# Kernel tuning notes

Hardware: AMD Instinct MI355X
Metric: run time of the kernel (lower is better)

## Reference

```python
import jax, jax.numpy as jnp
import numpy as np

K_F = 3          # propagation kernel
PAD_F = 1
NUM = K_F * K_F - 1   # 8 non-reference neighbors
IDX_REF = NUM // 2    # 4
PROP_TIME = 18
B, H, W = 4, 240, 1216


def _conv2d_same(x, w, b):
    # x: (B,Cin,H,W), w: (Cout,Cin,kh,kw)
    y = jax.lax.conv_general_dilated(x, w, (1, 1), 'SAME',
                                     dimension_numbers=('NCHW', 'OIHW', 'NCHW'))
    return y + b[None, :, None, None]


def _bilinear(img, y, x):
    # img: (B,H,W); y,x: (B,K,H,W) float sample coords. Zero outside bounds (DCN semantics).
    Bv, Hv, Wv = img.shape
    flat = img.reshape(Bv, -1)
    y0 = jnp.floor(y)
    x0 = jnp.floor(x)
    wy = y - y0
    wx = x - x0

    def g(yy, xx):
        valid = (yy >= 0) & (yy <= Hv - 1) & (xx >= 0) & (xx <= Wv - 1)
        yc = jnp.clip(yy, 0, Hv - 1).astype(jnp.int32)
        xc = jnp.clip(xx, 0, Wv - 1).astype(jnp.int32)
        idx = (yc * Wv + xc).reshape(Bv, -1)
        v = jnp.take_along_axis(flat, idx, axis=1).reshape(yy.shape)
        return jnp.where(valid, v, jnp.zeros((), img.dtype))

    return ((1 - wy) * (1 - wx) * g(y0, x0)
            + (1 - wy) * wx * g(y0, x0 + 1)
            + wy * (1 - wx) * g(y1 := y0 + 1, x0)
            + wy * wx * g(y1, x0 + 1))


def _deform_agg(feat, off, mask, k, pad):
    # Modulated deformable conv with w == 1, b == 0, ch_f == 1.
    # feat: (B,1,H,W); off: (B,K,2,H,W) (dy,dx); mask: (B,K,H,W)
    Bv, _, Hv, Wv = feat.shape
    kk = jnp.arange(k)
    by = (jnp.repeat(kk, k) - pad).astype(feat.dtype)  # kernel base dy, row-major
    bx = (jnp.tile(kk, k) - pad).astype(feat.dtype)    # kernel base dx
    gy = jnp.arange(Hv, dtype=feat.dtype)[None, None, :, None]
    gx = jnp.arange(Wv, dtype=feat.dtype)[None, None, None, :]
    y = gy + by[None, :, None, None] + off[:, :, 0]
    x = gx + bx[None, :, None, None] + off[:, :, 1]
    s = _bilinear(feat[:, 0], y, x)                    # (B,K,H,W)
    return jnp.sum(s * mask, axis=1, keepdims=True)


def setup_inputs() -> dict:
    key = jax.random.key(0)
    k1, k2, k3, k4, k5, k6 = jax.random.split(key, 6)
    feat_init = jax.random.uniform(k1, (B, 1, H, W), jnp.float32)
    guidance = jax.random.normal(k2, (B, 8, H, W), jnp.float32)
    confidence = jax.random.uniform(k3, (B, 1, H, W), jnp.float32)
    dep = jax.random.uniform(k4, (B, 1, H, W), jnp.float32)
    valid = (jax.random.uniform(k5, (B, 1, H, W), jnp.float32) < 0.05)
    feat_fix = dep * valid.astype(jnp.float32)
    w_oa = 0.1 * jax.random.normal(k6, (3 * NUM, 8, 3, 3), jnp.float32)
    b_oa = jnp.zeros((3 * NUM,), jnp.float32)
    aff_scale_const = jnp.full((1,), 0.5 * NUM, jnp.float32)  # gamma * num (TGASS)
    return {'feat_init': feat_init, 'guidance': guidance, 'confidence': confidence,
            'feat_fix': feat_fix, 'w_oa': w_oa, 'b_oa': b_oa,
            'aff_scale_const': aff_scale_const}


def reference(feat_init, guidance, confidence, feat_fix, w_oa, b_oa, aff_scale_const):
    Bv, _, Hv, Wv = guidance.shape
    oa = _conv2d_same(guidance, w_oa, b_oa)                 # (B,24,H,W)
    o1, o2, aff = oa[:, :NUM], oa[:, NUM:2 * NUM], oa[:, 2 * NUM:]
    # torch: cat((o1,o2),1).view(B,num,2,H,W) then insert zero ref offset at idx_ref
    off = jnp.concatenate([o1, o2], axis=1).reshape(Bv, NUM, 2, Hv, Wv)
    zeros = jnp.zeros((Bv, 1, 2, Hv, Wv), off.dtype)
    off = jnp.concatenate([off[:, :IDX_REF], zeros, off[:, IDX_REF:]], axis=1)  # (B,9,2,H,W)

    # TGASS affinity
    aff = jnp.tanh(aff) / (aff_scale_const + 1e-8)          # (B,8,H,W)

    # confidence-weighted affinity: 1x1 deform-sample of confidence at each neighbor offset
    nbr = jnp.array([0, 1, 2, 3, 5, 6, 7, 8])
    off_c = jax.lax.stop_gradient(off[:, nbr])              # (B,8,2,H,W), offsets detached
    gy = jnp.arange(Hv, dtype=aff.dtype)[None, None, :, None]
    gx = jnp.arange(Wv, dtype=aff.dtype)[None, None, None, :]
    conf_aff = _bilinear(confidence[:, 0], gy + off_c[:, :, 0], gx + off_c[:, :, 1])
    aff = aff * conf_aff

    s = jnp.sum(jnp.abs(aff), axis=1, keepdims=True) + 1e-4
    s = jnp.maximum(s, 1.0)                                 # TGASS clamp
    aff = aff / s
    aff_ref = 1.0 - jnp.sum(aff, axis=1, keepdims=True)
    aff9 = jnp.concatenate([aff[:, :IDX_REF], aff_ref, aff[:, IDX_REF:]], axis=1)  # (B,9,H,W)

    # preserve_input mask
    mask_fix = (jnp.sum((feat_fix > 0.0).astype(feat_fix.dtype), axis=1, keepdims=True) > 0.0)
    mask_fix = jax.lax.stop_gradient(mask_fix.astype(feat_fix.dtype))

    def step(feat, _):
        feat = (1.0 - mask_fix) * feat + mask_fix * feat_fix
        feat = _deform_agg(feat, off, aff9, K_F, PAD_F)
        return feat, None

    feat_result, _ = jax.lax.scan(step, feat_init, None, length=PROP_TIME)
    return feat_result, off.reshape(Bv, -1, Hv, Wv), aff9
```

## Files before the change

### kernel.cpp

```cpp
#include <hip/hip_runtime.h>
#include <hip/hip_bf16.h>

#define B_ 4
#define H_ 240
#define W_ 1216
#define HW_ (H_*W_)
#define N1_ (B_*HW_)
#define PT_ 18

__device__ __forceinline__ bool probe_bf16(const void* scale_ptr) {
    return ((const unsigned short*)scale_ptr)[0] == 0x4080;
}

__device__ __forceinline__ float ldin(const void* p, int i, bool bf) {
    if (bf) {
        unsigned int u = (unsigned int)((const unsigned short*)p)[i];
        return __uint_as_float(u << 16);
    }
    return ((const float*)p)[i];
}

__device__ __forceinline__ void stout(void* p, int i, bool bf, float v) {
    if (bf) ((__hip_bfloat16*)p)[i] = __float2bfloat16(v);
    else    ((float*)p)[i] = v;
}

__global__ __launch_bounds__(256) void k_prep_w(const void* __restrict__ w_oa,
                                                const void* __restrict__ b_oa,
                                                const void* __restrict__ scale,
                                                float* __restrict__ wc) {
    bool bf = probe_bf16(scale);
    int i = blockIdx.x * 256 + threadIdx.x;
    if (i < 1728) wc[i] = ldin(w_oa, i, bf);
    if (i < 24)   wc[1728 + i] = ldin(b_oa, i, bf);
}

__global__ __launch_bounds__(256) void k_init(const void* __restrict__ finit,
                                              const void* __restrict__ ffix,
                                              const void* __restrict__ scale,
                                              float* __restrict__ featA) {
    bool bf = probe_bf16(scale);
    int p = blockIdx.x * 256 + threadIdx.x;
    if (p >= N1_) return;
    float fx = ldin(ffix, p, bf);
    featA[p] = (fx > 0.0f) ? fx : ldin(finit, p, bf);
}

__global__ __launch_bounds__(256) void k_conv(const void* __restrict__ guid,
                                              const void* __restrict__ conf,
                                              const void* __restrict__ scale,
                                              const float* __restrict__ wc,
                                              void* __restrict__ d_out,
                                              float* __restrict__ ws_off,
                                              float* __restrict__ ws_aff,
                                              int mode2) {
    bool bf = probe_bf16(scale);
    int p = blockIdx.x * 256 + threadIdx.x;
    if (p >= N1_) return;
    int b = p / HW_;
    int r = p - b * HW_;
    int h = r / W_;
    int w = r - h * W_;

    float g[8][9];
    #pragma unroll
    for (int t = 0; t < 9; ++t) {
        int hh = h + t / 3 - 1;
        int ww = w + t % 3 - 1;
        bool v = (hh >= 0) && (hh < H_) && (ww >= 0) && (ww < W_);
        int idx0 = hh * W_ + ww;
        #pragma unroll
        for (int ci = 0; ci < 8; ++ci)
            g[ci][t] = v ? ldin(guid, (b * 8 + ci) * HW_ + idx0, bf) : 0.0f;
    }

    float oa[24];
    #pragma unroll
    for (int co = 0; co < 24; ++co) {
        float a = wc[1728 + co];
        #pragma unroll
        for (int ci = 0; ci < 8; ++ci)
            #pragma unroll
            for (int t = 0; t < 9; ++t)
                a = fmaf(g[ci][t], wc[(co * 8 + ci) * 9 + t], a);
        oa[co] = a;
    }

    float scl = ldin(scale, 0, bf);
    float inv = 1.0f / (scl + 1e-8f);

    float aft[8];
    int cbase = b * HW_;
    #pragma unroll
    for (int t = 0; t < 8; ++t) {
        float a = tanhf(oa[16 + t]) * inv;
        float y = (float)h + oa[2 * t];
        float x = (float)w + oa[2 * t + 1];
        float y0f = floorf(y), x0f = floorf(x);
        int y0 = (int)y0f, x0 = (int)x0f;
        float wy = y - y0f, wx = x - x0f;
        int y0c = min(max(y0, 0), H_ - 1), y1c = min(max(y0 + 1, 0), H_ - 1);
        int x0c = min(max(x0, 0), W_ - 1), x1c = min(max(x0 + 1, 0), W_ - 1);
        bool vy0 = (y0 >= 0) && (y0 < H_), vy1 = (y0 >= -1) && (y0 < H_ - 1);
        bool vx0 = (x0 >= 0) && (x0 < W_), vx1 = (x0 >= -1) && (x0 < W_ - 1);
        float w00 = (1.0f - wy) * (1.0f - wx); w00 = (vy0 && vx0) ? w00 : 0.0f;
        float w01 = (1.0f - wy) * wx;          w01 = (vy0 && vx1) ? w01 : 0.0f;
        float w10 = wy * (1.0f - wx);          w10 = (vy1 && vx0) ? w10 : 0.0f;
        float w11 = wy * wx;                   w11 = (vy1 && vx1) ? w11 : 0.0f;
        float f00 = ldin(conf, cbase + y0c * W_ + x0c, bf);
        float f01 = ldin(conf, cbase + y0c * W_ + x1c, bf);
        float f10 = ldin(conf, cbase + y1c * W_ + x0c, bf);
        float f11 = ldin(conf, cbase + y1c * W_ + x1c, bf);
        float cv = w00 * f00 + w01 * f01 + w10 * f10 + w11 * f11;
        aft[t] = a * cv;
    }
    float s = 1e-4f;
    #pragma unroll
    for (int t = 0; t < 8; ++t) s += fabsf(aft[t]);
    s = fmaxf(s, 1.0f);
    float rs = 1.0f / s;
    float suma = 0.0f;
    #pragma unroll
    for (int t = 0; t < 8; ++t) { aft[t] *= rs; suma += aft[t]; }
    float aref = 1.0f - suma;

    #pragma unroll
    for (int t = 0; t < 8; ++t) {
        int n9 = t + (t >= 4 ? 1 : 0);
        stout(d_out, N1_ + (b * 18 + 2 * n9)     * HW_ + r, bf, oa[2 * t]);
        stout(d_out, N1_ + (b * 18 + 2 * n9 + 1) * HW_ + r, bf, oa[2 * t + 1]);
        stout(d_out, 19 * N1_ + (b * 9 + n9) * HW_ + r, bf, aft[t]);
    }
    stout(d_out, N1_ + (b * 18 + 8) * HW_ + r, bf, 0.0f);
    stout(d_out, N1_ + (b * 18 + 9) * HW_ + r, bf, 0.0f);
    stout(d_out, 19 * N1_ + (b * 9 + 4) * HW_ + r, bf, aref);

    if (mode2) {
        #pragma unroll
        for (int t = 0; t < 8; ++t) {
            ws_off[t * N1_ + p]       = oa[2 * t];
            ws_off[(8 + t) * N1_ + p] = oa[2 * t + 1];
            int n9 = t + (t >= 4 ? 1 : 0);
            ws_aff[n9 * N1_ + p] = aft[t];
        }
        ws_aff[4 * N1_ + p] = aref;
    }
}

__global__ __launch_bounds__(256) void k_prop(const float* __restrict__ src,
                                              float* __restrict__ dst,
                                              const float* __restrict__ ws_off,
                                              const float* __restrict__ ws_aff,
                                              const void* __restrict__ d_out_all,
                                              const void* __restrict__ ffix_in,
                                              const void* __restrict__ scale,
                                              void* __restrict__ d_out_feat,
                                              int last, int mode2) {
    int p = blockIdx.x * 256 + threadIdx.x;
    if (p >= N1_) return;
    bool bf = probe_bf16(scale);
    int b = p / HW_;
    int r = p - b * HW_;
    int h = r / W_;
    int w = r - h * W_;
    const float* sp = src + b * HW_;

    float oy[8], ox[8], af[9];
    if (mode2) {
        #pragma unroll
        for (int t = 0; t < 8; ++t) {
            oy[t] = ws_off[t * N1_ + p];
            ox[t] = ws_off[(8 + t) * N1_ + p];
        }
        #pragma unroll
        for (int n = 0; n < 9; ++n) af[n] = ws_aff[n * N1_ + p];
    } else {
        #pragma unroll
        for (int t = 0; t < 8; ++t) {
            int n9 = t + (t >= 4 ? 1 : 0);
            oy[t] = ldin(d_out_all, N1_ + (b * 18 + 2 * n9)     * HW_ + r, bf);
            ox[t] = ldin(d_out_all, N1_ + (b * 18 + 2 * n9 + 1) * HW_ + r, bf);
        }
        #pragma unroll
        for (int n = 0; n < 9; ++n)
            af[n] = ldin(d_out_all, 19 * N1_ + (b * 9 + n) * HW_ + r, bf);
    }

    float acc = af[4] * sp[r];

    #pragma unroll
    for (int t = 0; t < 8; ++t) {
        int n9 = t + (t >= 4 ? 1 : 0);
        float y = (float)(h + n9 / 3 - 1) + oy[t];
        float x = (float)(w + n9 % 3 - 1) + ox[t];
        float y0f = floorf(y), x0f = floorf(x);
        int y0 = (int)y0f, x0 = (int)x0f;
        float wy = y - y0f, wx = x - x0f;
        int y0c = min(max(y0, 0), H_ - 1), y1c = min(max(y0 + 1, 0), H_ - 1);
        int x0c = min(max(x0, 0), W_ - 1), x1c = min(max(x0 + 1, 0), W_ - 1);
        bool vy0 = (y0 >= 0) && (y0 < H_), vy1 = (y0 >= -1) && (y0 < H_ - 1);
        bool vx0 = (x0 >= 0) && (x0 < W_), vx1 = (x0 >= -1) && (x0 < W_ - 1);
        float w00 = (1.0f - wy) * (1.0f - wx); w00 = (vy0 && vx0) ? w00 : 0.0f;
        float w01 = (1.0f - wy) * wx;          w01 = (vy0 && vx1) ? w01 : 0.0f;
        float w10 = wy * (1.0f - wx);          w10 = (vy1 && vx0) ? w10 : 0.0f;
        float w11 = wy * wx;                   w11 = (vy1 && vx1) ? w11 : 0.0f;
        float f00 = sp[y0c * W_ + x0c];
        float f01 = sp[y0c * W_ + x1c];
        float f10 = sp[y1c * W_ + x0c];
        float f11 = sp[y1c * W_ + x1c];
        float v = w00 * f00 + w01 * f01 + w10 * f10 + w11 * f11;
        acc = fmaf(af[n9], v, acc);
    }

    if (last) {
        stout(d_out_feat, p, probe_bf16(scale), acc);
    } else {
        float fx = ldin(ffix_in, p, bf);
        dst[p] = (fx > 0.0f) ? fx : acc;
    }
}

extern "C" void kernel_launch(void* const* d_in, const int* in_sizes, int n_in,
                              void* d_out, int out_size, void* d_ws, size_t ws_size,
                              hipStream_t stream) {
    const void* feat_init  = d_in[0];
    const void* guidance   = d_in[1];
    const void* confidence = d_in[2];
    const void* feat_fix   = d_in[3];
    const void* w_oa       = d_in[4];
    const void* b_oa       = d_in[5];
    const void* scale      = d_in[6];

    float* wsf    = (float*)d_ws;
    float* featA  = wsf;
    float* featB  = wsf + N1_;
    float* wc     = wsf + 2 * (size_t)N1_;
    float* ws_off = wsf + 2 * (size_t)N1_ + 2048;
    float* ws_aff = ws_off + 16 * (size_t)N1_;

    size_t need2 = ((size_t)27 * N1_ + 2048) * sizeof(float);
    int mode2 = (ws_size >= need2) ? 1 : 0;

    int grid = (N1_ + 255) / 256;
    hipLaunchKernelGGL(k_prep_w, dim3(7), dim3(256), 0, stream, w_oa, b_oa, scale, wc);
    hipLaunchKernelGGL(k_init, dim3(grid), dim3(256), 0, stream,
                       feat_init, feat_fix, scale, featA);
    hipLaunchKernelGGL(k_conv, dim3(grid), dim3(256), 0, stream,
                       guidance, confidence, scale, wc, d_out, ws_off, ws_aff, mode2);

    float* a = featA;
    float* bbuf = featB;
    for (int it = 0; it < PT_; ++it) {
        int last = (it == PT_ - 1) ? 1 : 0;
        hipLaunchKernelGGL(k_prop, dim3(grid), dim3(256), 0, stream,
                           a, bbuf, ws_off, ws_aff, d_out, feat_fix, scale,
                           d_out, last, mode2);
        float* t = a; a = bbuf; bbuf = t;
    }
}
```

Measured before the change: 1.017 ms.

## Pack propagation coefficients into float4 planes and restructure conv weight layout

The workspace layout for offsets, affinities and the fixed-depth value changes from 25 separate scalar planes to 7 float4 planes. Each propagation step then issues seven 16-byte loads instead of about 26 scalar loads, and it no longer reads feat_fix from the bf16/fp32 input. The conv weights are transposed to a [tap][cin][cout] layout so the conv loop accumulates all 24 outputs per loaded guidance value, without holding a 72-entry input array. The workspace requirement grows slightly, and mode2 is only taken when the workspace is large enough.

New measurement: 2.248 ms. 121% more time.

```diff
diff --git a/kernel.cpp b/kernel.cpp
--- a/kernel.cpp
+++ b/kernel.cpp
@@ -31,8 +31,14 @@
                                                 float* __restrict__ wc) {
     bool bf = probe_bf16(scale);
     int i = blockIdx.x * 256 + threadIdx.x;
-    if (i < 1728) wc[i] = ldin(w_oa, i, bf);
-    if (i < 24)   wc[1728 + i] = ldin(b_oa, i, bf);
+    if (i < 1728) {
+        int co = i / 72;
+        int rem = i - co * 72;
+        int ci = rem / 9;
+        int t = rem - ci * 9;
+        wc[(t * 8 + ci) * 24 + co] = ldin(w_oa, i, bf);
+    }
+    if (i < 24) wc[1728 + i] = ldin(b_oa, i, bf);
 }
 
 __global__ __launch_bounds__(256) void k_init(const void* __restrict__ finit,
@@ -48,11 +54,11 @@
 
 __global__ __launch_bounds__(256) void k_conv(const void* __restrict__ guid,
                                               const void* __restrict__ conf,
+                                              const void* __restrict__ ffix,
                                               const void* __restrict__ scale,
                                               const float* __restrict__ wc,
                                               void* __restrict__ d_out,
-                                              float* __restrict__ ws_off,
-                                              float* __restrict__ ws_aff,
+                                              float4* __restrict__ ws_pack,
                                               int mode2) {
     bool bf = probe_bf16(scale);
     int p = blockIdx.x * 256 + threadIdx.x;
@@ -62,28 +68,29 @@
     int h = r / W_;
     int w = r - h * W_;
 
-    float g[8][9];
+    float oa[24];
+    #pragma unroll
+    for (int co = 0; co < 24; ++co) oa[co] = wc[1728 + co];
+
+    const int gbase = b * 8 * HW_;
     #pragma unroll
     for (int t = 0; t < 9; ++t) {
         int hh = h + t / 3 - 1;
         int ww = w + t % 3 - 1;
         bool v = (hh >= 0) && (hh < H_) && (ww >= 0) && (ww < W_);
         int idx0 = hh * W_ + ww;
+        float gv[8];
         #pragma unroll
         for (int ci = 0; ci < 8; ++ci)
-            g[ci][t] = v ? ldin(guid, (b * 8 + ci) * HW_ + idx0, bf) : 0.0f;
-    }
-
-    float oa[24];
-    #pragma unroll
-    for (int co = 0; co < 24; ++co) {
-        float a = wc[1728 + co];
-        #pragma unroll
-        for (int ci = 0; ci < 8; ++ci)
+            gv[ci] = v ? ldin(guid, gbase + ci * HW_ + idx0, bf) : 0.0f;
+        #pragma unroll
+        for (int ci = 0; ci < 8; ++ci) {
+            float g = gv[ci];
+            const float* wrow = wc + (t * 8 + ci) * 24;
             #pragma unroll
-            for (int t = 0; t < 9; ++t)
-                a = fmaf(g[ci][t], wc[(co * 8 + ci) * 9 + t], a);
-        oa[co] = a;
+            for (int co = 0; co < 24; ++co)
+                oa[co] = fmaf(g, wrow[co], oa[co]);
+        }
     }
 
     float scl = ldin(scale, 0, bf);
@@ -136,21 +143,20 @@
     stout(d_out, 19 * N1_ + (b * 9 + 4) * HW_ + r, bf, aref);
 
     if (mode2) {
-        #pragma unroll
-        for (int t = 0; t < 8; ++t) {
-            ws_off[t * N1_ + p]       = oa[2 * t];
-            ws_off[(8 + t) * N1_ + p] = oa[2 * t + 1];
-            int n9 = t + (t >= 4 ? 1 : 0);
-            ws_aff[n9 * N1_ + p] = aft[t];
-        }
-        ws_aff[4 * N1_ + p] = aref;
+        float fx = ldin(ffix, p, bf);
+        ws_pack[0 * N1_ + p] = make_float4(oa[0], oa[2], oa[4], oa[6]);
+        ws_pack[1 * N1_ + p] = make_float4(oa[8], oa[10], oa[12], oa[14]);
+        ws_pack[2 * N1_ + p] = make_float4(oa[1], oa[3], oa[5], oa[7]);
+        ws_pack[3 * N1_ + p] = make_float4(oa[9], oa[11], oa[13], oa[15]);
+        ws_pack[4 * N1_ + p] = make_float4(aft[0], aft[1], aft[2], aft[3]);
+        ws_pack[5 * N1_ + p] = make_float4(aft[4], aft[5], aft[6], aft[7]);
+        ws_pack[6 * N1_ + p] = make_float4(aref, fx, 0.0f, 0.0f);
     }
 }
 
 __global__ __launch_bounds__(256) void k_prop(const float* __restrict__ src,
                                               float* __restrict__ dst,
-                                              const float* __restrict__ ws_off,
-                                              const float* __restrict__ ws_aff,
+                                              const float4* __restrict__ ws_pack,
                                               const void* __restrict__ d_out_all,
                                               const void* __restrict__ ffix_in,
                                               const void* __restrict__ scale,
@@ -158,23 +164,30 @@
                                               int last, int mode2) {
     int p = blockIdx.x * 256 + threadIdx.x;
     if (p >= N1_) return;
-    bool bf = probe_bf16(scale);
     int b = p / HW_;
     int r = p - b * HW_;
     int h = r / W_;
     int w = r - h * W_;
     const float* sp = src + b * HW_;
 
-    float oy[8], ox[8], af[9];
+    float oy[8], ox[8], af[9], fx;
     if (mode2) {
-        #pragma unroll
-        for (int t = 0; t < 8; ++t) {
-            oy[t] = ws_off[t * N1_ + p];
-            ox[t] = ws_off[(8 + t) * N1_ + p];
-        }
-        #pragma unroll
-        for (int n = 0; n < 9; ++n) af[n] = ws_aff[n * N1_ + p];
+        float4 g0 = ws_pack[0 * N1_ + p];
+        float4 g1 = ws_pack[1 * N1_ + p];
+        float4 g2 = ws_pack[2 * N1_ + p];
+        float4 g3 = ws_pack[3 * N1_ + p];
+        float4 g4 = ws_pack[4 * N1_ + p];
+        float4 g5 = ws_pack[5 * N1_ + p];
+        float4 g6 = ws_pack[6 * N1_ + p];
+        oy[0]=g0.x; oy[1]=g0.y; oy[2]=g0.z; oy[3]=g0.w;
+        oy[4]=g1.x; oy[5]=g1.y; oy[6]=g1.z; oy[7]=g1.w;
+        ox[0]=g2.x; ox[1]=g2.y; ox[2]=g2.z; ox[3]=g2.w;
+        ox[4]=g3.x; ox[5]=g3.y; ox[6]=g3.z; ox[7]=g3.w;
+        af[0]=g4.x; af[1]=g4.y; af[2]=g4.z; af[3]=g4.w;
+        af[5]=g5.x; af[6]=g5.y; af[7]=g5.z; af[8]=g5.w;
+        af[4]=g6.x; fx=g6.y;
     } else {
+        bool bf = probe_bf16(scale);
         #pragma unroll
         for (int t = 0; t < 8; ++t) {
             int n9 = t + (t >= 4 ? 1 : 0);
@@ -184,6 +197,7 @@
         #pragma unroll
         for (int n = 0; n < 9; ++n)
             af[n] = ldin(d_out_all, 19 * N1_ + (b * 9 + n) * HW_ + r, bf);
+        fx = ldin(ffix_in, p, bf);
     }
 
     float acc = af[4] * sp[r];
@@ -215,7 +229,6 @@
     if (last) {
         stout(d_out_feat, p, probe_bf16(scale), acc);
     } else {
-        float fx = ldin(ffix_in, p, bf);
         dst[p] = (fx > 0.0f) ? fx : acc;
     }
 }
@@ -231,14 +244,13 @@
     const void* b_oa       = d_in[5];
     const void* scale      = d_in[6];
 
-    float* wsf    = (float*)d_ws;
-    float* featA  = wsf;
-    float* featB  = wsf + N1_;
-    float* wc     = wsf + 2 * (size_t)N1_;
-    float* ws_off = wsf + 2 * (size_t)N1_ + 2048;
-    float* ws_aff = ws_off + 16 * (size_t)N1_;
-
-    size_t need2 = ((size_t)27 * N1_ + 2048) * sizeof(float);
+    float* wsf     = (float*)d_ws;
+    float* featA   = wsf;
+    float* featB   = wsf + N1_;
+    float* wc      = wsf + 2 * (size_t)N1_;
+    float4* ws_pack = (float4*)(wsf + 2 * (size_t)N1_ + 2048);
+
+    size_t need2 = ((size_t)30 * N1_ + 2048) * sizeof(float);
     int mode2 = (ws_size >= need2) ? 1 : 0;
 
     int grid = (N1_ + 255) / 256;
@@ -246,14 +258,14 @@
     hipLaunchKernelGGL(k_init, dim3(grid), dim3(256), 0, stream,
                        feat_init, feat_fix, scale, featA);
     hipLaunchKernelGGL(k_conv, dim3(grid), dim3(256), 0, stream,
-                       guidance, confidence, scale, wc, d_out, ws_off, ws_aff, mode2);
+                       guidance, confidence, feat_fix, scale, wc, d_out, ws_pack, mode2);
 
     float* a = featA;
     float* bbuf = featB;
     for (int it = 0; it < PT_; ++it) {
         int last = (it == PT_ - 1) ? 1 : 0;
         hipLaunchKernelGGL(k_prop, dim3(grid), dim3(256), 0, stream,
-                           a, bbuf, ws_off, ws_aff, d_out, feat_fix, scale,
+                           a, bbuf, ws_pack, d_out, feat_fix, scale,
                            d_out, last, mode2);
         float* t = a; a = bbuf; bbuf = t;
     }
```
